# Kernel optimization log

Hardware: AMD Instinct MI355X
Metric: run time of the kernel (lower is better)

The kernel has to match this reference:

```python
import jax, jax.numpy as jnp
import numpy as np
from functools import partial

POOL_H, POOL_W = 7, 7


def _bin_index(coord, start, stop, step, n_bins):
    """Map each pixel coordinate to its ROI-pool bin index (or n_bins if outside ROI).

    Bins i < n_bins-1 span [start + i*step, start + (i+1)*step); the last bin
    extends to `stop` (matching the original `(i+1)*h_step if i+1<pool_h else region_h`).
    coord: [L]; start/stop/step: [R] int32. Returns [R, L] int32 in [0, n_bins].
    """
    rel = coord[None, :] - start[:, None]                      # [R, L]
    idx = jnp.minimum(rel // jnp.maximum(step, 1)[:, None], n_bins - 1)
    idx = jnp.where(step[:, None] > 0, idx, n_bins - 1)        # step==0 -> all pixels in last bin
    valid = (rel >= 0) & (coord[None, :] < stop[:, None])
    return jnp.where(valid, idx, n_bins).astype(jnp.int32)


def _roi_pool_image(fm, rois, ph, pw):
    """fm: [H, W, C], rois: [R, 4] relative (h0, w0, h1, w1). Returns [R, ph, pw, C]."""
    H, W, C = fm.shape
    h0 = (H * rois[:, 0]).astype(jnp.int32)   # truncation == tf.cast(..., int32) for >=0
    w0 = (W * rois[:, 1]).astype(jnp.int32)
    h1 = (H * rois[:, 2]).astype(jnp.int32)
    w1 = (W * rois[:, 3]).astype(jnp.int32)
    h_step = (h1 - h0) // ph
    w_step = (w1 - w0) // pw

    idx_h = _bin_index(jnp.arange(H), h0, h1, h_step, ph)      # [R, H]
    idx_w = _bin_index(jnp.arange(W), w0, w1, w_step, pw)      # [R, W]

    neg = jnp.finfo(fm.dtype).min
    fm_whc = jnp.swapaxes(fm, 0, 1)                            # [W, H, C]

    def pool_one(ih, iw):
        # scatter-max columns into width bins (extra slot pw collects out-of-ROI pixels)
        t = jnp.full((pw + 1, H, C), neg, fm.dtype).at[iw].max(fm_whc)[:pw]  # [pw, H, C]
        # scatter-max rows into height bins
        o = jnp.full((ph + 1, pw, C), neg, fm.dtype).at[ih].max(jnp.swapaxes(t, 0, 1))[:ph]
        return o                                               # [ph, pw, C]

    return jax.vmap(pool_one)(idx_h, idx_w)


def setup_inputs() -> dict:
    key = jax.random.key(0)
    k1, k2, k3 = jax.random.split(key, 3)
    feature_map = jax.random.normal(k1, (2, 64, 64, 256), dtype=jnp.float32)
    starts = jax.random.uniform(k2, (2, 256, 2), minval=0.0, maxval=0.3)
    ends = jax.random.uniform(k3, (2, 256, 2), minval=0.6, maxval=1.0)
    rois = jnp.concatenate([starts, ends], axis=-1).astype(jnp.float32)  # (h0, w0, h1, w1)
    return {"feature_map": feature_map, "rois": rois}


def reference(feature_map, rois):
    # per-image ROI max pooling, vmapped over the batch -> [B, R, ph, pw, C]
    pool = partial(_roi_pool_image, ph=POOL_H, pw=POOL_W)
    return jax.vmap(pool)(feature_map, rois)
```

## Files before the change

### kernel.cpp

```cpp
#include <hip/hip_runtime.h>
#include <float.h>

constexpr int H = 64, W = 64, C = 256, PH = 7, PW = 7;

typedef float f32x4 __attribute__((ext_vector_type(4)));

__device__ __forceinline__ f32x4 vmax4(f32x4 a, f32x4 b) {
    f32x4 r;
    r.x = fmaxf(a.x, b.x); r.y = fmaxf(a.y, b.y);
    r.z = fmaxf(a.z, b.z); r.w = fmaxf(a.w, b.w);
    return r;
}

__device__ __forceinline__ void build_body(
    int bx, int lane, int wave,
    const float* __restrict__ fm, float* __restrict__ s4x,
    float* __restrict__ s4y, float* __restrict__ s4xy,
    f32x4 (*lds_fm)[64], f32x4 (*lds_sx)[64])
{
    const int x8 = bx & 7;
    const int z  = bx >> 3;
    const int b  = x8 >> 2;
    const int quart = x8 & 3;
    const int x  = z & (W - 1);
    const int y0 = quart * 16 + ((z >> 6) << 2);

    const int x1 = min(x + 1, W - 1), x2 = min(x + 2, W - 1), x3 = min(x + 3, W - 1);
    const float* fmb = fm + (size_t)b * H * W * C + (size_t)lane * 4;

    #pragma unroll
    for (int s = 0; s < 2; ++s) {
        const int slot = wave + 4 * s;
        if (slot < 7) {
            const int y = min(y0 + slot, H - 1);
            const float* row = fmb + (size_t)y * W * C;
            f32x4 v0 = *(const f32x4*)(row + (size_t)x  * C);
            f32x4 v1 = *(const f32x4*)(row + (size_t)x1 * C);
            f32x4 v2 = *(const f32x4*)(row + (size_t)x2 * C);
            f32x4 v3 = *(const f32x4*)(row + (size_t)x3 * C);
            lds_fm[slot][lane] = v0;
            lds_sx[slot][lane] = vmax4(vmax4(v0, v1), vmax4(v2, v3));
        }
    }
    __syncthreads();

    const int y = y0 + wave;
    const f32x4 sx = lds_sx[wave][lane];
    const f32x4 sy = vmax4(vmax4(lds_fm[wave][lane],     lds_fm[wave + 1][lane]),
                           vmax4(lds_fm[wave + 2][lane], lds_fm[wave + 3][lane]));
    const f32x4 sxy = vmax4(vmax4(lds_sx[wave][lane],     lds_sx[wave + 1][lane]),
                            vmax4(lds_sx[wave + 2][lane], lds_sx[wave + 3][lane]));

    const size_t o = ((size_t)(b * H + y) * W + x) * C + (size_t)lane * 4;
    *(f32x4*)(s4x  + o) = sx;
    *(f32x4*)(s4y  + o) = sy;
    *(f32x4*)(s4xy + o) = sxy;
}

__device__ __forceinline__ void query_unit(
    int x8, int n, int lane, int wave,
    const float* __restrict__ fm, const float* __restrict__ rois,
    const float* __restrict__ s4x, const float* __restrict__ s4y,
    const float* __restrict__ s4xy, float* __restrict__ out, int R,
    bool use_tables)
{
    const int b = x8 >> 2;
    const int g = x8 & 3;

    int i, id;
    if (g < 3) {
        i  = 2 * g + (n & 1);
        id = (n >> 1) * 4 + wave;
    } else {
        if (n >= 448) return;
        i  = 6;
        id = n * 4 + wave;
    }
    const int r = id / 7;
    const int j = id - 7 * r;

    const float* roi = rois + ((size_t)b * R + r) * 4;
    int h0 = (int)((float)H * roi[0]);
    int w0 = (int)((float)W * roi[1]);
    int h1 = (int)((float)H * roi[2]);
    int w1 = (int)((float)W * roi[3]);
    int hs = (h1 - h0) / PH;
    int ws = (w1 - w0) / PW;

    int ys, ye, xs, xe;
    if (hs > 0) { ys = h0 + i * hs; ye = (i < PH - 1) ? (ys + hs) : h1; }
    else        { ys = h0;          ye = (i == PH - 1) ? h1 : h0; }
    if (ws > 0) { xs = w0 + j * ws; xe = (j < PW - 1) ? (xs + ws) : w1; }
    else        { xs = w0;          xe = (j == PW - 1) ? w1 : w0; }
    ys = __builtin_amdgcn_readfirstlane(max(ys, 0));
    ye = __builtin_amdgcn_readfirstlane(min(ye, H));
    xs = __builtin_amdgcn_readfirstlane(max(xs, 0));
    xe = __builtin_amdgcn_readfirstlane(min(xe, W));

    const int hl = ye - ys, wl = xe - xs;
    const f32x4 NEG = {-FLT_MAX, -FLT_MAX, -FLT_MAX, -FLT_MAX};
    f32x4 a0 = NEG, a1 = NEG, a2 = NEG, a3 = NEG;

    if (use_tables) {
        if (hl > 0 && wl > 0) {
            const bool y4 = hl >= 4, x4 = wl >= 4;
            const int ny = y4 ? (hl + 3) >> 2 : hl;
            const int nx = x4 ? (wl + 3) >> 2 : wl;
            const int ystep = y4 ? 4 : 1, xstep = x4 ? 4 : 1;
            const int ycl = y4 ? ye - 4 : ye - 1;
            const int xcl = x4 ? xe - 4 : xe - 1;
            const float* tb = y4 ? (x4 ? s4xy : s4y) : (x4 ? s4x : fm);
            const float* tbb = tb + (size_t)b * H * W * C + lane * 4;

            const int xo0 = min(xs,             xcl) * C;
            const int xo1 = min(xs + xstep,     xcl) * C;
            const int xo2 = min(xs + 2 * xstep, xcl) * C;
            const int xo3 = min(xs + 3 * xstep, xcl) * C;

            #pragma unroll
            for (int ky = 0; ky < 4; ++ky) {
                if (ky < ny) {
                    const int y = min(ys + ystep * ky, ycl);
                    const float* rowp = tbb + (size_t)y * (W * C);
                    a0 = vmax4(a0, *(const f32x4*)(rowp + xo0));
                    if (nx > 1) a1 = vmax4(a1, *(const f32x4*)(rowp + xo1));
                    if (nx > 2) a2 = vmax4(a2, *(const f32x4*)(rowp + xo2));
                    if (nx > 3) a3 = vmax4(a3, *(const f32x4*)(rowp + xo3));
                }
            }
        }
    } else {
        const float* fmb2 = fm + (size_t)b * (H * W * C) + lane * 4;
        for (int y = ys; y < ye; y += 2) {
            const int yb = min(y + 1, ye - 1);
            const int ro0 = y  * (W * C);
            const int ro1 = yb * (W * C);
            for (int x = xs; x < xe; x += 2) {
                const int xb = min(x + 1, xe - 1);
                a0 = vmax4(a0, *(const f32x4*)(fmb2 + ro0 + x  * C));
                a1 = vmax4(a1, *(const f32x4*)(fmb2 + ro0 + xb * C));
                a2 = vmax4(a2, *(const f32x4*)(fmb2 + ro1 + x  * C));
                a3 = vmax4(a3, *(const f32x4*)(fmb2 + ro1 + xb * C));
            }
        }
    }
    const f32x4 acc = vmax4(vmax4(a0, a1), vmax4(a2, a3));

    size_t o = ((((size_t)b * R + r) * PH + i) * PW + j) * C + (size_t)lane * 4;
    __builtin_nontemporal_store(acc, reinterpret_cast<f32x4*>(out + o));
}

__global__ __launch_bounds__(256, 8) void roi_pool_fused2(
    const float* __restrict__ fm, const float* __restrict__ rois,
    float* __restrict__ s4x, float* __restrict__ s4y, float* __restrict__ s4xy,
    float* __restrict__ out, int R, unsigned* __restrict__ cnt)
{
    __shared__ f32x4 lds_fm[7][64];
    __shared__ f32x4 lds_sx[7][64];
    __shared__ int s_ok;

    const int lane = threadIdx.x & 63;
    const int wave = __builtin_amdgcn_readfirstlane(threadIdx.x >> 6);

    build_body(blockIdx.x, lane, wave, fm, s4x, s4y, s4xy, lds_fm, lds_sx);

    __threadfence();
    const int cls = blockIdx.x & 7;
    const int b   = cls >> 2;
    if (threadIdx.x == 0) {
        __hip_atomic_fetch_add(&cnt[cls * 32], 1u,
                               __ATOMIC_RELEASE, __HIP_MEMORY_SCOPE_AGENT);
        int ok = 1;
        #pragma unroll
        for (int c = 0; c < 4; ++c) {
            const unsigned* p = &cnt[(b * 4 + c) * 32];
            int spins = 0;
            while (__hip_atomic_load(p, __ATOMIC_RELAXED,
                                     __HIP_MEMORY_SCOPE_AGENT) < 256u) {
                __builtin_amdgcn_s_sleep(2);
                if (++spins > (1 << 18)) { ok = 0; break; }
            }
            if (!ok) break;
        }
        s_ok = ok;
    }
    __syncthreads();
    __threadfence();
    const bool use_tables = (s_ok != 0);

    const int base = blockIdx.x >> 3;
    #pragma unroll
    for (int k = 0; k < 4; ++k) {
        const int n = base + 256 * k;
        if (n < 896)
            query_unit(cls, n, lane, wave, fm, rois, s4x, s4y, s4xy, out, R,
                       use_tables);
    }
}

__global__ __launch_bounds__(256) void build_tables(
    const float* __restrict__ fm, float* __restrict__ s4x,
    float* __restrict__ s4y, float* __restrict__ s4xy)
{
    __shared__ f32x4 lds_fm[7][64];
    __shared__ f32x4 lds_sx[7][64];
    const int lane = threadIdx.x & 63;
    const int wave = __builtin_amdgcn_readfirstlane(threadIdx.x >> 6);
    build_body(blockIdx.x, lane, wave, fm, s4x, s4y, s4xy, lds_fm, lds_sx);
}

__global__ __launch_bounds__(256) void roi_pool_q(
    const float* __restrict__ fm, const float* __restrict__ rois,
    const float* __restrict__ s4x, const float* __restrict__ s4y,
    const float* __restrict__ s4xy, float* __restrict__ out, int R)
{
    const int lane = threadIdx.x & 63;
    const int wave = __builtin_amdgcn_readfirstlane(threadIdx.x >> 6);
    query_unit(blockIdx.x & 7, blockIdx.x >> 3, lane, wave,
               fm, rois, s4x, s4y, s4xy, out, R, true);
}

__global__ __launch_bounds__(256) void roi_pool_direct(
    const float* __restrict__ fm, const float* __restrict__ rois,
    float* __restrict__ out, int R)
{
    const int lane = threadIdx.x & 63;
    const int wave = __builtin_amdgcn_readfirstlane(threadIdx.x >> 6);
    const int b = blockIdx.x & 1;
    int m = (blockIdx.x >> 1) * 4 + wave;
    int j = m % PW; m /= PW;
    int i = m % PH; m /= PH;
    int r = m;

    const float* roi = rois + ((size_t)b * R + r) * 4;
    int h0 = (int)((float)H * roi[0]);
    int w0 = (int)((float)W * roi[1]);
    int h1 = (int)((float)H * roi[2]);
    int w1 = (int)((float)W * roi[3]);
    int hs = (h1 - h0) / PH;
    int ws = (w1 - w0) / PW;

    int ys, ye, xs, xe;
    if (hs > 0) { ys = h0 + i * hs; ye = (i < PH - 1) ? (ys + hs) : h1; }
    else        { ys = h0;          ye = (i == PH - 1) ? h1 : h0; }
    if (ws > 0) { xs = w0 + j * ws; xe = (j < PW - 1) ? (xs + ws) : w1; }
    else        { xs = w0;          xe = (j == PW - 1) ? w1 : w0; }
    ys = __builtin_amdgcn_readfirstlane(max(ys, 0));
    ye = __builtin_amdgcn_readfirstlane(min(ye, H));
    xs = __builtin_amdgcn_readfirstlane(max(xs, 0));
    xe = __builtin_amdgcn_readfirstlane(min(xe, W));

    const f32x4 NEG = {-FLT_MAX, -FLT_MAX, -FLT_MAX, -FLT_MAX};
    f32x4 a0 = NEG, a1 = NEG, a2 = NEG, a3 = NEG;
    const float* fmb = fm + (size_t)b * (H * W * C);
    const int lo = lane * 4;

    for (int y = ys; y < ye; y += 2) {
        const int y1 = min(y + 1, ye - 1);
        const int ro0 = y  * (W * C);
        const int ro1 = y1 * (W * C);
        for (int x = xs; x < xe; x += 2) {
            const int x1 = min(x + 1, xe - 1);
            a0 = vmax4(a0, *(const f32x4*)(fmb + ro0 + x  * C + lo));
            a1 = vmax4(a1, *(const f32x4*)(fmb + ro0 + x1 * C + lo));
            a2 = vmax4(a2, *(const f32x4*)(fmb + ro1 + x  * C + lo));
            a3 = vmax4(a3, *(const f32x4*)(fmb + ro1 + x1 * C + lo));
        }
    }
    f32x4 acc = vmax4(vmax4(a0, a1), vmax4(a2, a3));
    size_t o = ((((size_t)b * R + r) * PH + i) * PW + j) * C + (size_t)lo;
    __builtin_nontemporal_store(acc, reinterpret_cast<f32x4*>(out + o));
}

extern "C" void kernel_launch(void* const* d_in, const int* in_sizes, int n_in,
                              void* d_out, int out_size, void* d_ws, size_t ws_size,
                              hipStream_t stream) {
    const float* fm   = (const float*)d_in[0];
    const float* rois = (const float*)d_in[1];
    float* out = (float*)d_out;

    const int B = in_sizes[0] / (H * W * C);
    const int R = in_sizes[1] / (B * 4);

    const size_t tbl = (size_t)B * H * W * C;
    const size_t need = 3 * tbl * sizeof(float);

    if (B == 2 && R == 256 && ws_size >= need + 4096) {
        float* s4x  = (float*)d_ws;
        float* s4y  = s4x + tbl;
        float* s4xy = s4y + tbl;
        unsigned* cnt = (unsigned*)((char*)d_ws + need);

        int nb = 0;
        hipError_t oe = hipOccupancyMaxActiveBlocksPerMultiprocessor(
            &nb, roi_pool_fused2, 256, 0);

        if (oe == hipSuccess && nb >= 8) {
            hipMemsetAsync(cnt, 0, 8 * 32 * sizeof(unsigned), stream);
            roi_pool_fused2<<<2048, 256, 0, stream>>>(
                fm, rois, s4x, s4y, s4xy, out, R, cnt);
        } else {
            build_tables<<<2048, 256, 0, stream>>>(fm, s4x, s4y, s4xy);
            roi_pool_q  <<<7168, 256, 0, stream>>>(fm, rois, s4x, s4y, s4xy, out, R);
        }
    } else {
        const int qblocks = B * (R * PH * PW / 4);
        roi_pool_direct<<<qblocks, 256, 0, stream>>>(fm, rois, out, R);
    }
}
```

Baseline: 24.26 us.

## Wait only on table quarters each wave's bins need, per-wave spin

The fused kernel previously had thread 0 spin until all four row-quarter table builds for its image had finished, then broadcast through LDS and a block barrier. Now each wave first computes bounds for its bins, builds a mask of the 16-row quarters those bins touch, and spins only on those counters. This drops the block-wide barrier and lets waves start as soon as their dependencies are ready. In exchange, every wave issues its own atomic polling, and the spin timeout is halved.

```diff
diff --git a/kernel.cpp b/kernel.cpp
--- a/kernel.cpp
+++ b/kernel.cpp
@@ -57,28 +57,10 @@
     *(f32x4*)(s4xy + o) = sxy;
 }
 
-__device__ __forceinline__ void query_unit(
-    int x8, int n, int lane, int wave,
-    const float* __restrict__ fm, const float* __restrict__ rois,
-    const float* __restrict__ s4x, const float* __restrict__ s4y,
-    const float* __restrict__ s4xy, float* __restrict__ out, int R,
-    bool use_tables)
-{
-    const int b = x8 >> 2;
-    const int g = x8 & 3;
-
-    int i, id;
-    if (g < 3) {
-        i  = 2 * g + (n & 1);
-        id = (n >> 1) * 4 + wave;
-    } else {
-        if (n >= 448) return;
-        i  = 6;
-        id = n * 4 + wave;
-    }
-    const int r = id / 7;
-    const int j = id - 7 * r;
-
+__device__ __forceinline__ void bin_bounds(
+    const float* __restrict__ rois, int b, int R, int r, int i, int j,
+    int& ys, int& ye, int& xs, int& xe)
+{
     const float* roi = rois + ((size_t)b * R + r) * 4;
     int h0 = (int)((float)H * roi[0]);
     int w0 = (int)((float)W * roi[1]);
@@ -87,7 +69,6 @@
     int hs = (h1 - h0) / PH;
     int ws = (w1 - w0) / PW;
 
-    int ys, ye, xs, xe;
     if (hs > 0) { ys = h0 + i * hs; ye = (i < PH - 1) ? (ys + hs) : h1; }
     else        { ys = h0;          ye = (i == PH - 1) ? h1 : h0; }
     if (ws > 0) { xs = w0 + j * ws; xe = (j < PW - 1) ? (xs + ws) : w1; }
@@ -96,13 +77,19 @@
     ye = __builtin_amdgcn_readfirstlane(min(ye, H));
     xs = __builtin_amdgcn_readfirstlane(max(xs, 0));
     xe = __builtin_amdgcn_readfirstlane(min(xe, W));
-
+}
+
+__device__ __forceinline__ f32x4 gather_bin(
+    int b, int lane, int ys, int ye, int xs, int xe, bool use_tables,
+    const float* __restrict__ fm, const float* __restrict__ s4x,
+    const float* __restrict__ s4y, const float* __restrict__ s4xy)
+{
     const int hl = ye - ys, wl = xe - xs;
     const f32x4 NEG = {-FLT_MAX, -FLT_MAX, -FLT_MAX, -FLT_MAX};
     f32x4 a0 = NEG, a1 = NEG, a2 = NEG, a3 = NEG;
 
-    if (use_tables) {
-        if (hl > 0 && wl > 0) {
+    if (hl > 0 && wl > 0) {
+        if (use_tables) {
             const bool y4 = hl >= 4, x4 = wl >= 4;
             const int ny = y4 ? (hl + 3) >> 2 : hl;
             const int nx = x4 ? (wl + 3) >> 2 : wl;
@@ -128,36 +115,32 @@
                     if (nx > 3) a3 = vmax4(a3, *(const f32x4*)(rowp + xo3));
                 }
             }
-        }
-    } else {
-        const float* fmb2 = fm + (size_t)b * (H * W * C) + lane * 4;
-        for (int y = ys; y < ye; y += 2) {
-            const int yb = min(y + 1, ye - 1);
-            const int ro0 = y  * (W * C);
-            const int ro1 = yb * (W * C);
-            for (int x = xs; x < xe; x += 2) {
-                const int xb = min(x + 1, xe - 1);
-                a0 = vmax4(a0, *(const f32x4*)(fmb2 + ro0 + x  * C));
-                a1 = vmax4(a1, *(const f32x4*)(fmb2 + ro0 + xb * C));
-                a2 = vmax4(a2, *(const f32x4*)(fmb2 + ro1 + x  * C));
-                a3 = vmax4(a3, *(const f32x4*)(fmb2 + ro1 + xb * C));
+        } else {
+            const float* fmb2 = fm + (size_t)b * (H * W * C) + lane * 4;
+            for (int y = ys; y < ye; y += 2) {
+                const int yb = min(y + 1, ye - 1);
+                const int ro0 = y  * (W * C);
+                const int ro1 = yb * (W * C);
+                for (int x = xs; x < xe; x += 2) {
+                    const int xb = min(x + 1, xe - 1);
+                    a0 = vmax4(a0, *(const f32x4*)(fmb2 + ro0 + x  * C));
+                    a1 = vmax4(a1, *(const f32x4*)(fmb2 + ro0 + xb * C));
+                    a2 = vmax4(a2, *(const f32x4*)(fmb2 + ro1 + x  * C));
+                    a3 = vmax4(a3, *(const f32x4*)(fmb2 + ro1 + xb * C));
+                }
             }
         }
     }
-    const f32x4 acc = vmax4(vmax4(a0, a1), vmax4(a2, a3));
-
-    size_t o = ((((size_t)b * R + r) * PH + i) * PW + j) * C + (size_t)lane * 4;
-    __builtin_nontemporal_store(acc, reinterpret_cast<f32x4*>(out + o));
-}
-
-__global__ __launch_bounds__(256, 8) void roi_pool_fused2(
+    return vmax4(vmax4(a0, a1), vmax4(a2, a3));
+}
+
+__global__ __launch_bounds__(256, 8) void roi_pool_fused3(
     const float* __restrict__ fm, const float* __restrict__ rois,
     float* __restrict__ s4x, float* __restrict__ s4y, float* __restrict__ s4xy,
     float* __restrict__ out, int R, unsigned* __restrict__ cnt)
 {
     __shared__ f32x4 lds_fm[7][64];
     __shared__ f32x4 lds_sx[7][64];
-    __shared__ int s_ok;
 
     const int lane = threadIdx.x & 63;
     const int wave = __builtin_amdgcn_readfirstlane(threadIdx.x >> 6);
@@ -167,34 +150,62 @@
     __threadfence();
     const int cls = blockIdx.x & 7;
     const int b   = cls >> 2;
-    if (threadIdx.x == 0) {
+    if (threadIdx.x == 0)
         __hip_atomic_fetch_add(&cnt[cls * 32], 1u,
                                __ATOMIC_RELEASE, __HIP_MEMORY_SCOPE_AGENT);
-        int ok = 1;
-        #pragma unroll
-        for (int c = 0; c < 4; ++c) {
-            const unsigned* p = &cnt[(b * 4 + c) * 32];
+
+    const int g    = cls & 3;
+    const int base = blockIdx.x >> 3;
+
+    int u_ys[4], u_ye[4], u_xs[4], u_xe[4], u_i[4], u_r[4];
+    bool u_ok[4];
+    unsigned qmask = 0;
+    #pragma unroll
+    for (int k = 0; k < 4; ++k) {
+        const int n = base + 256 * k;
+        bool valid;
+        int i, id;
+        if (g < 3) { valid = (n < 896); i = 2 * g + (n & 1); id = (n >> 1) * 4 + wave; }
+        else       { valid = (n < 448); i = 6;               id = n * 4 + wave; }
+        u_ok[k] = valid;
+        if (valid) {
+            const int r = id / 7;
+            u_r[k] = r; u_i[k] = i;
+            bin_bounds(rois, b, R, r, i, id - 7 * r,
+                       u_ys[k], u_ye[k], u_xs[k], u_xe[k]);
+            if (u_ye[k] > u_ys[k] && u_xe[k] > u_xs[k]) {
+                const int q0 = u_ys[k] >> 4, q1 = (u_ye[k] - 1) >> 4;
+                qmask |= ((1u << (q1 + 1)) - (1u << q0));
+            }
+        }
+    }
+
+    bool tables_ok = true;
+    #pragma unroll
+    for (int q = 0; q < 4; ++q) {
+        if (qmask & (1u << q)) {
+            const unsigned* p = &cnt[(b * 4 + q) * 32];
             int spins = 0;
             while (__hip_atomic_load(p, __ATOMIC_RELAXED,
                                      __HIP_MEMORY_SCOPE_AGENT) < 256u) {
                 __builtin_amdgcn_s_sleep(2);
-                if (++spins > (1 << 18)) { ok = 0; break; }
+                if (++spins > (1 << 17)) { tables_ok = false; break; }
             }
-            if (!ok) break;
-        }
-        s_ok = ok;
-    }
-    __syncthreads();
+        }
+    }
     __threadfence();
-    const bool use_tables = (s_ok != 0);
-
-    const int base = blockIdx.x >> 3;
+
     #pragma unroll
     for (int k = 0; k < 4; ++k) {
-        const int n = base + 256 * k;
-        if (n < 896)
-            query_unit(cls, n, lane, wave, fm, rois, s4x, s4y, s4xy, out, R,
-                       use_tables);
+        if (u_ok[k]) {
+            const f32x4 acc = gather_bin(b, lane, u_ys[k], u_ye[k], u_xs[k],
+                                         u_xe[k], tables_ok, fm, s4x, s4y, s4xy);
+            const int n = base + 256 * k;
+            const int j = ((g < 3) ? ((n >> 1) * 4 + wave) : (n * 4 + wave)) - 7 * u_r[k];
+            size_t o = ((((size_t)b * R + u_r[k]) * PH + u_i[k]) * PW + j) * C
+                       + (size_t)lane * 4;
+            __builtin_nontemporal_store(acc, reinterpret_cast<f32x4*>(out + o));
+        }
     }
 }
 
@@ -216,8 +227,23 @@
 {
     const int lane = threadIdx.x & 63;
     const int wave = __builtin_amdgcn_readfirstlane(threadIdx.x >> 6);
-    query_unit(blockIdx.x & 7, blockIdx.x >> 3, lane, wave,
-               fm, rois, s4x, s4y, s4xy, out, R, true);
+    const int x8 = blockIdx.x & 7;
+    const int n  = blockIdx.x >> 3;
+    const int b  = x8 >> 2;
+    const int g  = x8 & 3;
+
+    int i, id;
+    if (g < 3) { i = 2 * g + (n & 1); id = (n >> 1) * 4 + wave; }
+    else       { if (n >= 448) return; i = 6; id = n * 4 + wave; }
+    const int r = id / 7;
+    const int j = id - 7 * r;
+
+    int ys, ye, xs, xe;
+    bin_bounds(rois, b, R, r, i, j, ys, ye, xs, xe);
+    const f32x4 acc = gather_bin(b, lane, ys, ye, xs, xe, true,
+                                 fm, s4x, s4y, s4xy);
+    size_t o = ((((size_t)b * R + r) * PH + i) * PW + j) * C + (size_t)lane * 4;
+    __builtin_nontemporal_store(acc, reinterpret_cast<f32x4*>(out + o));
 }
 
 __global__ __launch_bounds__(256) void roi_pool_direct(
@@ -232,43 +258,11 @@
     int i = m % PH; m /= PH;
     int r = m;
 
-    const float* roi = rois + ((size_t)b * R + r) * 4;
-    int h0 = (int)((float)H * roi[0]);
-    int w0 = (int)((float)W * roi[1]);
-    int h1 = (int)((float)H * roi[2]);
-    int w1 = (int)((float)W * roi[3]);
-    int hs = (h1 - h0) / PH;
-    int ws = (w1 - w0) / PW;
-
     int ys, ye, xs, xe;
-    if (hs > 0) { ys = h0 + i * hs; ye = (i < PH - 1) ? (ys + hs) : h1; }
-    else        { ys = h0;          ye = (i == PH - 1) ? h1 : h0; }
-    if (ws > 0) { xs = w0 + j * ws; xe = (j < PW - 1) ? (xs + ws) : w1; }
-    else        { xs = w0;          xe = (j == PW - 1) ? w1 : w0; }
-    ys = __builtin_amdgcn_readfirstlane(max(ys, 0));
-    ye = __builtin_amdgcn_readfirstlane(min(ye, H));
-    xs = __builtin_amdgcn_readfirstlane(max(xs, 0));
-    xe = __builtin_amdgcn_readfirstlane(min(xe, W));
-
-    const f32x4 NEG = {-FLT_MAX, -FLT_MAX, -FLT_MAX, -FLT_MAX};
-    f32x4 a0 = NEG, a1 = NEG, a2 = NEG, a3 = NEG;
-    const float* fmb = fm + (size_t)b * (H * W * C);
-    const int lo = lane * 4;
-
-    for (int y = ys; y < ye; y += 2) {
-        const int y1 = min(y + 1, ye - 1);
-        const int ro0 = y  * (W * C);
-        const int ro1 = y1 * (W * C);
-        for (int x = xs; x < xe; x += 2) {
-            const int x1 = min(x + 1, xe - 1);
-            a0 = vmax4(a0, *(const f32x4*)(fmb + ro0 + x  * C + lo));
-            a1 = vmax4(a1, *(const f32x4*)(fmb + ro0 + x1 * C + lo));
-            a2 = vmax4(a2, *(const f32x4*)(fmb + ro1 + x  * C + lo));
-            a3 = vmax4(a3, *(const f32x4*)(fmb + ro1 + x1 * C + lo));
-        }
-    }
-    f32x4 acc = vmax4(vmax4(a0, a1), vmax4(a2, a3));
-    size_t o = ((((size_t)b * R + r) * PH + i) * PW + j) * C + (size_t)lo;
+    bin_bounds(rois, b, R, r, i, j, ys, ye, xs, xe);
+    const f32x4 acc = gather_bin(b, lane, ys, ye, xs, xe, false,
+                                 fm, nullptr, nullptr, nullptr);
+    size_t o = ((((size_t)b * R + r) * PH + i) * PW + j) * C + (size_t)lane * 4;
     __builtin_nontemporal_store(acc, reinterpret_cast<f32x4*>(out + o));
 }
 
@@ -293,11 +287,11 @@
 
         int nb = 0;
         hipError_t oe = hipOccupancyMaxActiveBlocksPerMultiprocessor(
-            &nb, roi_pool_fused2, 256, 0);
+            &nb, roi_pool_fused3, 256, 0);
 
         if (oe == hipSuccess && nb >= 8) {
             hipMemsetAsync(cnt, 0, 8 * 32 * sizeof(unsigned), stream);
-            roi_pool_fused2<<<2048, 256, 0, stream>>>(
+            roi_pool_fused3<<<2048, 256, 0, stream>>>(
                 fm, rois, s4x, s4y, s4xy, out, R, cnt);
         } else {
             build_tables<<<2048, 256, 0, stream>>>(fm, s4x, s4y, s4xy);
```

Measured after the change: 24.35 us. About the same (+0.4%).
